# Optimization experiments

Measured on AMD Instinct MI355X. Metric: run time of the kernel, lower is better.

The kernel has to match this reference:

```python
import jax, jax.numpy as jnp
import numpy as np

N = 1_000_000   # memory slots (current_size == memory_size)
D = 64          # embedding_dim == compressed_dim (required by the source code)
B = 64          # query batch
QBITS = 8       # quantization_bits


def setup_inputs() -> dict:
    key = jax.random.key(0)
    ks = jax.random.split(key, 6)
    return {
        "query": jax.random.normal(ks[0], (B, D), dtype=jnp.float32),
        "memory": jax.random.normal(ks[1], (N, D), dtype=jnp.float32),
        "attention_weights": jax.random.normal(ks[2], (N,), dtype=jnp.float32),
        "Wq": jax.random.normal(ks[3], (D, D), dtype=jnp.float32) / np.sqrt(D),
        "Wk": jax.random.normal(ks[4], (D, D), dtype=jnp.float32) / np.sqrt(D),
        "Wv": jax.random.normal(ks[5], (D, D), dtype=jnp.float32) / np.sqrt(D),
        "top_k": 5,
    }


def reference(query, memory, attention_weights, Wq, Wk, Wv, top_k):
    d = memory.shape[1]
    levels = jnp.float32(2 ** QBITS - 1)
    # _quantize_tensor / _dequantize_tensor round-trip on the stored memory
    mn = memory.min()
    mx = memory.max()
    scale = (mx - mn) / levels
    zero_point = -mn / scale
    mem_dq = (jnp.round(memory / scale + zero_point) - zero_point) * scale  # [N, D]

    q = query @ Wq.T                    # [B, D]
    keys = mem_dq @ Wk.T                # [N, D]
    values = mem_dq @ Wv.T              # [N, D]

    # attention scores + per-slot bias
    scores = q @ keys.T / np.float32(np.sqrt(d)) + attention_weights[None, :]  # [B, N]

    top_scores, top_idx = jax.lax.top_k(scores, top_k)   # [B, k]
    gathered = jnp.take(values, top_idx, axis=0)         # [B, k, D] irregular gather
    dist = jax.nn.softmax(top_scores, axis=-1)           # [B, k]
    out = jnp.einsum('bk,bkd->bd', dist, gathered)       # [B, D]
    return out
```

## Files before the change

kernel.cpp:

```cpp
#include <hip/hip_runtime.h>
#include <stdint.h>

constexpr int NROWS = 1000000;
constexpr int D = 64;
constexpr int B = 64;
constexpr int TOPK = 5;
constexpr int TBLK = 4;
constexpr int TRES = 16;
constexpr int NB2MAX = 1024;

typedef __attribute__((ext_vector_type(8))) short short8;
typedef __attribute__((ext_vector_type(4))) float floatx4;
typedef __attribute__((ext_vector_type(4))) unsigned uintx4;
typedef unsigned long long u64;

#define OFF_QKF   512
#define OFF_QKB   16896
#define OFF_MM    25088
#define OFF_CAND  57856

__device__ __forceinline__ unsigned fkey(float x) {
    unsigned u = __float_as_uint(x);
    return (u & 0x80000000u) ? ~u : (u | 0x80000000u);
}
__device__ __forceinline__ float fkey_inv(unsigned k) {
    unsigned u = (k & 0x80000000u) ? (k ^ 0x80000000u) : ~k;
    return __uint_as_float(u);
}
__device__ __forceinline__ unsigned short f2bf_rne(float x) {
    unsigned u = __float_as_uint(x);
    u += 0x7fffu + ((u >> 16) & 1u);
    return (unsigned short)(u >> 16);
}
__device__ __forceinline__ unsigned pack_bf16(float lo, float hi) {
    return (__float_as_uint(hi) & 0xFFFF0000u) | (__float_as_uint(lo) >> 16);
}

template<int K>
__device__ __forceinline__ void insert_key(u64 (&ks)[K], u64 key) {
    if (key > ks[K - 1]) {
        #pragma unroll
        for (int j = K - 1; j > 0; --j)
            ks[j] = (key > ks[j - 1]) ? ks[j - 1] : ((key > ks[j]) ? key : ks[j]);
        ks[0] = (key > ks[0]) ? key : ks[0];
    }
}

__device__ __forceinline__ void insert2u(unsigned& a, unsigned& b, unsigned key) {
    unsigned lo = a < key ? a : key;
    unsigned hi = a < key ? key : a;
    a = hi;
    b = b < lo ? lo : b;
}

__device__ __forceinline__ u64 expand_key(unsigned k32, int wbeg) {
    if (!k32) return 0ull;
    unsigned row = (unsigned)wbeg + (0xFFFu - (k32 & 0xFFFu));
    return ((u64)(k32 & 0xFFFFF000u) << 32) | (unsigned)~row;
}

__global__ void k_qk(const float* __restrict__ query, const float* __restrict__ Wq,
                     const float* __restrict__ Wk,
                     float* __restrict__ qkf, unsigned short* __restrict__ qkb) {
    __shared__ float q[4][64];
    int t = threadIdx.x;
    int b0 = blockIdx.x * 4;
    int bq = t >> 6, d = t & 63;
    float s1 = 0.f;
    for (int e = 0; e < 64; e++) s1 += query[(b0 + bq) * 64 + e] * Wq[d * 64 + e];
    q[bq][d] = s1;
    __syncthreads();
    float v = 0.f;
    for (int dd = 0; dd < 64; dd++) v += q[bq][dd] * Wk[dd * 64 + d];
    v *= 0.125f;
    qkf[(b0 + bq) * 64 + d] = v;
    qkb[(b0 + bq) * 64 + d] = f2bf_rne(v);
}

__device__ __forceinline__ void proc_tile(
        const float4& T0, const float4& T1, const float4& T2, const float4& T3,
        const float4& TA, int it, int qr,
        const short8 (&bq)[4][2], unsigned (&Ltop)[4], unsigned (&Lsec)[4],
        float& mnv, float& mxv) {
    mnv = fminf(mnv, fminf(fminf(T0.x, T0.y), fminf(T0.z, T0.w)));
    mxv = fmaxf(mxv, fmaxf(fmaxf(T0.x, T0.y), fmaxf(T0.z, T0.w)));
    mnv = fminf(mnv, fminf(fminf(T1.x, T1.y), fminf(T1.z, T1.w)));
    mxv = fmaxf(mxv, fmaxf(fmaxf(T1.x, T1.y), fmaxf(T1.z, T1.w)));
    mnv = fminf(mnv, fminf(fminf(T2.x, T2.y), fminf(T2.z, T2.w)));
    mxv = fmaxf(mxv, fmaxf(fmaxf(T2.x, T2.y), fmaxf(T2.z, T2.w)));
    mnv = fminf(mnv, fminf(fminf(T3.x, T3.y), fminf(T3.z, T3.w)));
    mxv = fmaxf(mxv, fmaxf(fmaxf(T3.x, T3.y), fmaxf(T3.z, T3.w)));

    uintx4 ua0 = { pack_bf16(T0.x, T0.y), pack_bf16(T0.z, T0.w),
                   pack_bf16(T1.x, T1.y), pack_bf16(T1.z, T1.w) };
    uintx4 ua1 = { pack_bf16(T2.x, T2.y), pack_bf16(T2.z, T2.w),
                   pack_bf16(T3.x, T3.y), pack_bf16(T3.z, T3.w) };
    short8 a0 = __builtin_bit_cast(short8, ua0);
    short8 a1 = __builtin_bit_cast(short8, ua1);

    int idb = 0xFFF - it * 16 - qr;
    #pragma unroll
    for (int bt = 0; bt < 4; bt++) {
        floatx4 acc = {TA.x, TA.y, TA.z, TA.w};
        acc = __builtin_amdgcn_mfma_f32_16x16x32_bf16(a0, bq[bt][0], acc, 0, 0, 0);
        acc = __builtin_amdgcn_mfma_f32_16x16x32_bf16(a1, bq[bt][1], acc, 0, 0, 0);
        #pragma unroll
        for (int r = 0; r < 4; r++) {
            unsigned kk = (fkey(acc[r]) & 0xFFFFF000u) | (unsigned)(idb - r);
            insert2u(Ltop[bt], Lsec[bt], kk);
        }
    }
}

__launch_bounds__(256, 4)
__global__ void k_score_mm(const float* __restrict__ mem, const float* __restrict__ aw,
                           const unsigned short* __restrict__ qkb,
                           u64* __restrict__ cand,
                           unsigned* __restrict__ part, int wrows) {
    __shared__ u64 mrg[4][4][16][2];
    __shared__ float swmn[4], swmx[4];

    int t = threadIdx.x;
    int l15 = t & 15, quad = (t >> 4) & 3, w = t >> 6;
    int qr = quad * 4;

    short8 bq[4][2];
    #pragma unroll
    for (int bt = 0; bt < 4; bt++) {
        #pragma unroll
        for (int kb = 0; kb < 2; kb++)
            bq[bt][kb] = *(const short8*)(qkb + (bt * 16 + l15) * 64 + quad * 16 + kb * 8);
    }

    unsigned Ltop[4], Lsec[4];
    #pragma unroll
    for (int bt = 0; bt < 4; bt++) { Ltop[bt] = 0u; Lsec[bt] = 0u; }

    float mnv = 3.402823466e38f, mxv = -3.402823466e38f;

    int gw = blockIdx.x * 4 + w;
    int wbeg = gw * wrows;
    int wend = min(wbeg + wrows, NROWS);
    int span = wend - wbeg;
    int nt = span > 0 ? (span >> 4) : 0;

    const char* pbase = (const char*)mem + (size_t)wbeg * 256 + (size_t)(l15 * 256 + quad * 64);
    const float* abase = aw + wbeg + qr;

    float4 A0, A1, A2, A3, AA, B0, B1, B2, B3, BA;

#define LOADT(T0, T1, T2, T3, TA, TILE) do {                                   \
        const char* pn_ = pbase + (size_t)(TILE) * 4096;                       \
        T0 = *(const float4*)(pn_);                                            \
        T1 = *(const float4*)(pn_ + 16);                                       \
        T2 = *(const float4*)(pn_ + 32);                                       \
        T3 = *(const float4*)(pn_ + 48);                                       \
        TA = *(const float4*)(abase + (TILE) * 16);                            \
    } while (0)

    if (nt > 0) {
        LOADT(A0, A1, A2, A3, AA, 0);
        for (int it = 0; it < nt; it += 2) {
            LOADT(B0, B1, B2, B3, BA, it + 1);
            proc_tile(A0, A1, A2, A3, AA, it, qr, bq, Ltop, Lsec, mnv, mxv);
            int nx = (it + 2 < nt) ? it + 2 : nt - 1;
            LOADT(A0, A1, A2, A3, AA, nx);
            proc_tile(B0, B1, B2, B3, BA, it + 1, qr, bq, Ltop, Lsec, mnv, mxv);
        }
    }
#undef LOADT

    #pragma unroll
    for (int o = 32; o > 0; o >>= 1) {
        mnv = fminf(mnv, __shfl_xor(mnv, o));
        mxv = fmaxf(mxv, __shfl_xor(mxv, o));
    }
    if ((t & 63) == 0) { swmn[w] = mnv; swmx[w] = mxv; }

    #pragma unroll
    for (int bt = 0; bt < 4; bt++) {
        #pragma unroll
        for (int dlt = 16; dlt <= 32; dlt <<= 1) {
            unsigned ka = __shfl_xor(Ltop[bt], dlt);
            unsigned kb = __shfl_xor(Lsec[bt], dlt);
            insert2u(Ltop[bt], Lsec[bt], ka);
            insert2u(Ltop[bt], Lsec[bt], kb);
        }
    }
    if ((t & 48) == 0) {
        #pragma unroll
        for (int bt = 0; bt < 4; bt++) {
            mrg[w][bt][l15][0] = expand_key(Ltop[bt], wbeg);
            mrg[w][bt][l15][1] = expand_key(Lsec[bt], wbeg);
        }
    }
    __syncthreads();

    if (t == 0) {
        float a = fminf(fminf(swmn[0], swmn[1]), fminf(swmn[2], swmn[3]));
        float b2 = fmaxf(fmaxf(swmx[0], swmx[1]), fmaxf(swmx[2], swmx[3]));
        part[blockIdx.x * 2 + 0] = fkey(a);
        part[blockIdx.x * 2 + 1] = fkey(b2);
    }
    if (t < 64) {
        u64 ts[TBLK];
        #pragma unroll
        for (int j = 0; j < TBLK; j++) ts[j] = 0ull;
        int bt = t >> 4, l = t & 15;
        #pragma unroll
        for (int w2 = 0; w2 < 4; w2++) {
            insert_key<TBLK>(ts, mrg[w2][bt][l][0]);
            insert_key<TBLK>(ts, mrg[w2][bt][l][1]);
        }
        #pragma unroll
        for (int j = 0; j < TBLK; j++)
            cand[((long long)blockIdx.x * 64 + t) * TBLK + j] = ts[j];
    }
}

__global__ void k_finalize(const u64* __restrict__ cand, int nb2,
                           const float* __restrict__ mem, const float* __restrict__ aw,
                           const float* __restrict__ Wv, const unsigned* __restrict__ part,
                           const float* __restrict__ qkf, float* __restrict__ out) {
    __shared__ u64 lists[256][TRES];
    __shared__ float qkr[64];
    __shared__ int exid[TRES];
    __shared__ u64 exkey[TRES];
    __shared__ float exsc[TRES];
    __shared__ float wsel[TOPK];
    __shared__ int isel[TOPK];
    __shared__ float su[64];
    __shared__ unsigned redmn[4], redmx[4];
    __shared__ float sscale[2];

    int t = threadIdx.x, b = blockIdx.x;
    int total = nb2 * TBLK;

    unsigned mnk = 0xFFFFFFFFu, mxk = 0u;
    for (int i = t; i < nb2; i += 256) {
        unsigned a = part[2 * i], c = part[2 * i + 1];
        mnk = a < mnk ? a : mnk;
        mxk = c > mxk ? c : mxk;
    }
    #pragma unroll
    for (int o = 32; o > 0; o >>= 1) {
        unsigned am = __shfl_xor(mnk, o); mnk = am < mnk ? am : mnk;
        unsigned ax = __shfl_xor(mxk, o); mxk = ax > mxk ? ax : mxk;
    }
    int w4 = t >> 6;
    if ((t & 63) == 0) { redmn[w4] = mnk; redmx[w4] = mxk; }

    u64 loc[TRES];
    #pragma unroll
    for (int j = 0; j < TRES; j++) loc[j] = 0ull;
    for (int i = t; i < total; i += 256) {
        int blk = i / TBLK, j = i - blk * TBLK;
        insert_key<TRES>(loc, cand[((long long)blk * 64 + b) * TBLK + j]);
    }
    #pragma unroll
    for (int j = 0; j < TRES; j++) lists[t][j] = loc[j];
    if (t < 64) qkr[t] = qkf[b * 64 + t];
    __syncthreads();

    if (t == 255) {
        unsigned m0 = redmn[0], M0 = redmx[0];
        #pragma unroll
        for (int i = 1; i < 4; i++) {
            m0 = redmn[i] < m0 ? redmn[i] : m0;
            M0 = redmx[i] > M0 ? redmx[i] : M0;
        }
        float mnv = fkey_inv(m0), mxv = fkey_inv(M0);
        float scale = (mxv - mnv) / 255.0f;
        sscale[0] = scale;
        sscale[1] = -mnv / scale;
    }

    for (int s = 128; s > 0; s >>= 1) {
        if (t < s) {
            #pragma unroll
            for (int j = 0; j < TRES; j++) insert_key<TRES>(loc, lists[t + s][j]);
            #pragma unroll
            for (int j = 0; j < TRES; j++) lists[t][j] = loc[j];
        }
        __syncthreads();
    }
    if (t < TRES) {
        u64 k = lists[0][t];
        exid[t] = k ? (int)(~(unsigned)k) : 0;
    }
    __syncthreads();

    float scale = sscale[0], zp = sscale[1];

    int lane = t & 63, w = t >> 6;
    for (int i = 0; i < 4; i++) {
        int c = w * 4 + i;
        int idx = exid[c];
        float m = mem[(long long)idx * 64 + lane];
        float dq = (rintf(m / scale + zp) - zp) * scale;
        float p2 = dq * qkr[lane];
        for (int o = 32; o > 0; o >>= 1) p2 += __shfl_xor(p2, o);
        if (lane == 0) {
            float ex = p2 + aw[idx];
            exsc[c] = ex;
            exkey[c] = ((u64)fkey(ex) << 32) | (unsigned)(~(unsigned)idx);
        }
    }
    __syncthreads();

    if (t == 0) {
        u64 bnd = ~0ull;
        float ssel[TOPK];
        for (int p = 0; p < TOPK; p++) {
            u64 best = 0ull; int bc = 0;
            for (int c = 0; c < TRES; c++) {
                u64 k = exkey[c];
                if (k < bnd && k > best) { best = k; bc = c; }
            }
            bnd = best;
            ssel[p] = exsc[bc];
            isel[p] = exid[bc];
        }
        float Z = 0.f;
        for (int p = 0; p < TOPK; p++) { wsel[p] = expf(ssel[p] - ssel[0]); Z += wsel[p]; }
        for (int p = 0; p < TOPK; p++) wsel[p] /= Z;
    }
    __syncthreads();

    if (t < 64) {
        float u = 0.f;
        #pragma unroll
        for (int p = 0; p < TOPK; p++) {
            float m = mem[(long long)isel[p] * 64 + t];
            float dq = (rintf(m / scale + zp) - zp) * scale;
            u += wsel[p] * dq;
        }
        su[t] = u;
    }
    __syncthreads();
    if (t < 64) {
        float o = 0.f;
        #pragma unroll
        for (int e = 0; e < 64; e++) o += su[e] * Wv[t * 64 + e];
        out[b * 64 + t] = o;
    }
}

extern "C" void kernel_launch(void* const* d_in, const int* in_sizes, int n_in,
                              void* d_out, int out_size, void* d_ws, size_t ws_size,
                              hipStream_t stream) {
    const float* query = (const float*)d_in[0];
    const float* mem   = (const float*)d_in[1];
    const float* aw    = (const float*)d_in[2];
    const float* Wq    = (const float*)d_in[3];
    const float* Wk    = (const float*)d_in[4];
    const float* Wv    = (const float*)d_in[5];
    float* out = (float*)d_out;

    char* ws = (char*)d_ws;
    float* qkf     = (float*)(ws + OFF_QKF);
    unsigned short* qkb = (unsigned short*)(ws + OFF_QKB);
    unsigned* part = (unsigned*)(ws + OFF_MM);
    u64* cand = (u64*)(ws + OFF_CAND);

    int nb2 = NB2MAX;
    size_t need = (size_t)OFF_CAND + (size_t)nb2 * 64 * TBLK * 8;
    if (ws_size < need) {
        size_t avail = ws_size > OFF_CAND ? ws_size - OFF_CAND : 0;
        nb2 = (int)(avail / ((size_t)64 * TBLK * 8));
        if (nb2 < 64) nb2 = 64;
        if (nb2 > NB2MAX) nb2 = NB2MAX;
    }
    int waves = nb2 * 4;
    int wrows = ((NROWS + waves - 1) / waves + 31) / 32 * 32;

    k_qk<<<16, 256, 0, stream>>>(query, Wq, Wk, qkf, qkb);
    k_score_mm<<<nb2, 256, 0, stream>>>(mem, aw, qkb, cand, part, wrows);
    k_finalize<<<B, 256, 0, stream>>>(cand, nb2, mem, aw, Wv, part, qkf, out);
}
```

Baseline: 414.6 us.

## Transpose candidate layout, split MFMA chains, cache Wq in LDS, retune grid

The candidate buffer is stored query-major, so each finalize block now reads a contiguous slice instead of a strided gather. The two dependent MFMAs per tile are split into independent accumulators and summed afterwards, shortening the dependency chain. k_qk stages Wq in padded shared memory to get coalesced loads. The grid shrinks from 1024 to 768 blocks and the launch bound drops from 4 to 3 blocks per SM, giving more registers per thread but lower occupancy.

```diff
diff --git a/kernel.cpp b/kernel.cpp
--- a/kernel.cpp
+++ b/kernel.cpp
@@ -7,7 +7,7 @@
 constexpr int TOPK = 5;
 constexpr int TBLK = 4;
 constexpr int TRES = 16;
-constexpr int NB2MAX = 1024;
+constexpr int NB2MAX = 768;
 
 typedef __attribute__((ext_vector_type(8))) short short8;
 typedef __attribute__((ext_vector_type(4))) float floatx4;
@@ -62,12 +62,24 @@
 __global__ void k_qk(const float* __restrict__ query, const float* __restrict__ Wq,
                      const float* __restrict__ Wk,
                      float* __restrict__ qkf, unsigned short* __restrict__ qkb) {
+    __shared__ float wq[64][65];
     __shared__ float q[4][64];
     int t = threadIdx.x;
     int b0 = blockIdx.x * 4;
     int bq = t >> 6, d = t & 63;
+
+    #pragma unroll
+    for (int i = 0; i < 4; i++) {
+        int flat = (i * 256 + t) * 4;
+        float4 v = *(const float4*)(Wq + flat);
+        int r = flat >> 6, c = flat & 63;
+        wq[r][c + 0] = v.x; wq[r][c + 1] = v.y;
+        wq[r][c + 2] = v.z; wq[r][c + 3] = v.w;
+    }
+    __syncthreads();
+
     float s1 = 0.f;
-    for (int e = 0; e < 64; e++) s1 += query[(b0 + bq) * 64 + e] * Wq[d * 64 + e];
+    for (int e = 0; e < 64; e++) s1 += query[(b0 + bq) * 64 + e] * wq[d][e];
     q[bq][d] = s1;
     __syncthreads();
     float v = 0.f;
@@ -98,24 +110,25 @@
     short8 a0 = __builtin_bit_cast(short8, ua0);
     short8 a1 = __builtin_bit_cast(short8, ua1);
 
+    floatx4 zero = {0.f, 0.f, 0.f, 0.f};
     int idb = 0xFFF - it * 16 - qr;
     #pragma unroll
     for (int bt = 0; bt < 4; bt++) {
-        floatx4 acc = {TA.x, TA.y, TA.z, TA.w};
-        acc = __builtin_amdgcn_mfma_f32_16x16x32_bf16(a0, bq[bt][0], acc, 0, 0, 0);
-        acc = __builtin_amdgcn_mfma_f32_16x16x32_bf16(a1, bq[bt][1], acc, 0, 0, 0);
+        floatx4 acc0 = {TA.x, TA.y, TA.z, TA.w};
+        acc0 = __builtin_amdgcn_mfma_f32_16x16x32_bf16(a0, bq[bt][0], acc0, 0, 0, 0);
+        floatx4 acc1 = __builtin_amdgcn_mfma_f32_16x16x32_bf16(a1, bq[bt][1], zero, 0, 0, 0);
         #pragma unroll
         for (int r = 0; r < 4; r++) {
-            unsigned kk = (fkey(acc[r]) & 0xFFFFF000u) | (unsigned)(idb - r);
+            unsigned kk = (fkey(acc0[r] + acc1[r]) & 0xFFFFF000u) | (unsigned)(idb - r);
             insert2u(Ltop[bt], Lsec[bt], kk);
         }
     }
 }
 
-__launch_bounds__(256, 4)
+__launch_bounds__(256, 3)
 __global__ void k_score_mm(const float* __restrict__ mem, const float* __restrict__ aw,
                            const unsigned short* __restrict__ qkb,
-                           u64* __restrict__ cand,
+                           u64* __restrict__ cand, int nb2,
                            unsigned* __restrict__ part, int wrows) {
     __shared__ u64 mrg[4][4][16][2];
     __shared__ float swmn[4], swmx[4];
@@ -214,7 +227,7 @@
         }
         #pragma unroll
         for (int j = 0; j < TBLK; j++)
-            cand[((long long)blockIdx.x * 64 + t) * TBLK + j] = ts[j];
+            cand[((long long)t * nb2 + blockIdx.x) * TBLK + j] = ts[j];
     }
 }
 
@@ -250,13 +263,12 @@
     int w4 = t >> 6;
     if ((t & 63) == 0) { redmn[w4] = mnk; redmx[w4] = mxk; }
 
+    const u64* cb = cand + (long long)b * total;
     u64 loc[TRES];
     #pragma unroll
     for (int j = 0; j < TRES; j++) loc[j] = 0ull;
-    for (int i = t; i < total; i += 256) {
-        int blk = i / TBLK, j = i - blk * TBLK;
-        insert_key<TRES>(loc, cand[((long long)blk * 64 + b) * TBLK + j]);
-    }
+    for (int i = t; i < total; i += 256)
+        insert_key<TRES>(loc, cb[i]);
     #pragma unroll
     for (int j = 0; j < TRES; j++) lists[t][j] = loc[j];
     if (t < 64) qkr[t] = qkf[b * 64 + t];
@@ -375,6 +387,6 @@
     int wrows = ((NROWS + waves - 1) / waves + 31) / 32 * 32;
 
     k_qk<<<16, 256, 0, stream>>>(query, Wq, Wk, qkf, qkb);
-    k_score_mm<<<nb2, 256, 0, stream>>>(mem, aw, qkb, cand, part, wrows);
+    k_score_mm<<<nb2, 256, 0, stream>>>(mem, aw, qkb, cand, nb2, part, wrows);
     k_finalize<<<B, 256, 0, stream>>>(cand, nb2, mem, aw, Wv, part, qkf, out);
 }
```

New measurement: 408.5 us. Within noise of the previous version (-1.5%).
